# Kernel tuning notes

Measured on AMD Instinct MI355X. Metric: run time of the kernel, lower is better.

The kernel has to match this reference:

```python
import jax, jax.numpy as jnp
import numpy as np

FACTOR = 5  # sampling factor c

def setup_inputs() -> dict:
    key = jax.random.key(0)
    k1, k2, k3, k4 = jax.random.split(key, 4)
    B, H, L, D = 4, 8, 2048, 64
    u = min(max(1, FACTOR * int(np.ceil(np.log(L)))), L)  # sample_k = 40
    return {
        "queries": jax.random.normal(k1, (B, H, L, D), jnp.float32),
        "keys": jax.random.normal(k2, (B, H, L, D), jnp.float32),
        "values": jax.random.normal(k3, (B, H, L, D), jnp.float32),
        "index_sample": jax.random.randint(k4, (L, u), 0, L, jnp.int32),
    }

def reference(queries, keys, values, index_sample):
    B, H, L_Q, D = queries.shape
    L_K = keys.shape[2]
    scale = 1.0 / np.sqrt(D)
    U_part = min(max(1, FACTOR * int(np.ceil(np.log(L_K)))), L_Q)  # n_top queries

    # --- _prob_QK: sampled scores + sparsity measure ---
    # K_sample[b,h,q,s,:] = keys[b,h,index_sample[q,s],:]  -> (B,H,L_Q,u,D)
    K_sample = keys[:, :, index_sample, :]
    QK_sample = jnp.einsum('bhqd,bhqsd->bhqs', queries, K_sample)  # (B,H,L_Q,u)
    M = QK_sample.max(-1) - QK_sample.sum(-1) / L_K                # (B,H,L_Q)
    _, index = jax.lax.top_k(M, U_part)                            # (B,H,U)

    # --- initial context: mean of V for non-selected queries ---
    context = jnp.broadcast_to(values.mean(-2, keepdims=True), (B, H, L_Q, D))

    # --- full attention for the top-U queries only ---
    Q_reduce = jnp.take_along_axis(queries, index[..., None], axis=2)   # (B,H,U,D)
    scores = jnp.einsum('bhud,bhkd->bhuk', Q_reduce, keys) * scale      # (B,H,U,L_K)
    attn = jax.nn.softmax(scores, axis=-1)
    out = jnp.einsum('bhuk,bhkd->bhud', attn, values)                   # (B,H,U,D)

    # --- scatter selected outputs back into the mean context ---
    bi = jnp.arange(B)[:, None, None]
    hi = jnp.arange(H)[None, :, None]
    context = context.at[bi, hi, index].set(out)
    return context
```

## Files before the change

### kernel.cpp

```cpp
#include <hip/hip_runtime.h>
#include <math.h>

#define Bq 4
#define Hh 8
#define Lh 2048
#define Dh 64
#define BH (Bq*Hh)

__global__ __launch_bounds__(256) void kAC(const float* __restrict__ Q,
                                           const float* __restrict__ K,
                                           const float* __restrict__ V,
                                           const int* __restrict__ idxs,
                                           float2* __restrict__ M2,
                                           float* __restrict__ vpart, int u) {
    int bi = blockIdx.x;
    int tid = threadIdx.x;
    if (bi < 2048) {
        int xcd = bi & 7, slot = bi >> 3;
        int bh  = xcd * 4 + (slot >> 6);
        int qt  = (slot >> 1) & 31;
        int half = slot & 1;
        int wave = tid >> 6, lane = tid & 63;
        int g = lane >> 2, c = lane & 3;
        int q = qt * 64 + wave * 16 + g;
        long gq = (long)bh * Lh + q;

        const float* qrow = Q + gq * Dh;
        float4 qf[4];
#pragma unroll
        for (int jj = 0; jj < 4; ++jj)
            qf[jj] = *(const float4*)(qrow + jj * 16 + c * 4);

        int cnt1 = u >> 1;
        int c0 = (half == 0) ? (u - cnt1) : cnt1;
        const int* irow = idxs + (long)q * u + (half ? (u - cnt1) : 0);
        const float* kbase = K + (long)bh * Lh * Dh;

        float mx = -INFINITY, sm = 0.f;
        int s = 0;
        for (; s + 4 <= c0; s += 4) {
            int i0 = irow[s], i1 = irow[s+1], i2 = irow[s+2], i3 = irow[s+3];
            const float* kp0 = kbase + (long)i0 * Dh + c * 4;
            const float* kp1 = kbase + (long)i1 * Dh + c * 4;
            const float* kp2 = kbase + (long)i2 * Dh + c * 4;
            const float* kp3 = kbase + (long)i3 * Dh + c * 4;
            float4 kf[4][4];
#pragma unroll
            for (int jj = 0; jj < 4; ++jj) {
                kf[0][jj] = *(const float4*)(kp0 + jj * 16);
                kf[1][jj] = *(const float4*)(kp1 + jj * 16);
                kf[2][jj] = *(const float4*)(kp2 + jj * 16);
                kf[3][jj] = *(const float4*)(kp3 + jj * 16);
            }
            float a[4];
#pragma unroll
            for (int r = 0; r < 4; ++r) {
                float ac = 0.f;
#pragma unroll
                for (int jj = 0; jj < 4; ++jj)
                    ac += qf[jj].x*kf[r][jj].x + qf[jj].y*kf[r][jj].y
                        + qf[jj].z*kf[r][jj].z + qf[jj].w*kf[r][jj].w;
                a[r] = ac;
            }
#pragma unroll
            for (int r = 0; r < 4; ++r) {
                a[r] += __shfl_xor(a[r], 1);
                a[r] += __shfl_xor(a[r], 2);
                mx = fmaxf(mx, a[r]); sm += a[r];
            }
        }
        for (; s < c0; ++s) {
            int ki = irow[s];
            const float* krow = kbase + (long)ki * Dh + c * 4;
            float acc = 0.f;
#pragma unroll
            for (int jj = 0; jj < 4; ++jj) {
                float4 kf = *(const float4*)(krow + jj * 16);
                acc += qf[jj].x*kf.x + qf[jj].y*kf.y + qf[jj].z*kf.z + qf[jj].w*kf.w;
            }
            acc += __shfl_xor(acc, 1);
            acc += __shfl_xor(acc, 2);
            mx = fmaxf(mx, acc); sm += acc;
        }
        if (c == 0) M2[gq * 2 + half] = make_float2(mx, sm);
    } else {
        int b2 = bi - 2048;
        int xcd = b2 & 7, slot = b2 >> 3;
        int bh = xcd * 4 + (slot >> 3);
        int chunk = slot & 7;
        int d = tid & 63, r0 = tid >> 6;
        const float* vb = V + ((long)bh * Lh + chunk * 256) * Dh;
        float s = 0.f;
        for (int i = 0; i < 64; ++i) s += vb[(r0 + 4 * i) * Dh + d];
        __shared__ float part[4][64];
        part[r0][d] = s;
        __syncthreads();
        if (tid < 64) {
            float t = part[0][tid] + part[1][tid] + part[2][tid] + part[3][tid];
            vpart[(bh * 8 + chunk) * 64 + tid] = t;
        }
    }
}

__global__ __launch_bounds__(256) void kBE(const float2* __restrict__ M2,
                                           const float* __restrict__ vpart,
                                           int* __restrict__ topk,
                                           float* __restrict__ ctx, int U) {
    int bi = blockIdx.x;
    int tid = threadIdx.x;
    if (bi < 4096) {
        long base = (long)bi * 1024;
        int bh = (int)(base >> 17);
        __shared__ float vm[64];
        if (tid < 64) {
            float s = 0.f;
#pragma unroll
            for (int c2 = 0; c2 < 8; ++c2) s += vpart[(bh * 8 + c2) * 64 + tid];
            vm[tid] = s * (1.0f / (float)Lh);
        }
        __syncthreads();
        float4 val = *(const float4*)(vm + ((tid * 4) & 63));
        *(float4*)(ctx + base + tid * 4) = val;
        return;
    }
    int bh = bi - 4096;
    unsigned key[8];
#pragma unroll
    for (int j = 0; j < 8; ++j) {
        long q = (long)bh * Lh + tid + 256 * j;
        float4 mm = *(const float4*)(&M2[q * 2]);
        float Mv = fmaxf(mm.x, mm.z) - (mm.y + mm.w) * (1.0f / (float)Lh);
        unsigned ub = __float_as_uint(Mv);
        key[j] = ub ^ ((ub >> 31) ? 0xFFFFFFFFu : 0x80000000u);
    }
    __shared__ unsigned hist[256];
    __shared__ unsigned prefix_s;
    __shared__ int need_s;
    if (tid == 0) { prefix_s = 0u; need_s = U; }

    for (int level = 3; level >= 0; --level) {
        int shift = level * 8;
        hist[tid] = 0u;
        __syncthreads();
        unsigned prefix = prefix_s;
        int need = need_s;
        unsigned pmask = (level == 3) ? 0u : (0xFFFFFFFFu << (shift + 8));
#pragma unroll
        for (int j = 0; j < 8; ++j)
            if ((key[j] & pmask) == prefix)
                atomicAdd(&hist[(key[j] >> shift) & 0xFF], 1u);
        __syncthreads();
        if (tid < 64) {
            int lane = tid;
            unsigned h0 = hist[lane*4+0], h1 = hist[lane*4+1],
                     h2 = hist[lane*4+2], h3 = hist[lane*4+3];
            unsigned lt = h0 + h1 + h2 + h3;
            unsigned ssum = lt;
#pragma unroll
            for (int off = 1; off < 64; off <<= 1) {
                unsigned t = __shfl_down(ssum, off);
                if (lane + off < 64) ssum += t;
            }
            unsigned sx  = ssum - lt;
            unsigned suf3 = sx  + h3;
            unsigned suf2 = suf3 + h2;
            unsigned suf1 = suf2 + h1;
            unsigned suf0 = suf1 + h0;
            int localb = -1; unsigned nxt = 0u;
            if      ((int)suf3 >= need) { localb = lane*4+3; nxt = sx;   }
            else if ((int)suf2 >= need) { localb = lane*4+2; nxt = suf3; }
            else if ((int)suf1 >= need) { localb = lane*4+1; nxt = suf2; }
            else if ((int)suf0 >= need) { localb = lane*4+0; nxt = suf1; }
            unsigned long long ball = __ballot(localb >= 0);
            int hilane = 63 - __clzll(ball);
            if (lane == hilane) {
                prefix_s = prefix | ((unsigned)localb << shift);
                need_s = need - (int)nxt;
            }
        }
        __syncthreads();
    }
    unsigned T = prefix_s;
    int r = need_s;
    __shared__ int cgt, ceq;
    if (tid == 0) { cgt = 0; ceq = 0; }
    __syncthreads();
    int* out = topk + bh * U;
#pragma unroll
    for (int j = 0; j < 8; ++j) {
        if (key[j] > T) { int p = atomicAdd(&cgt, 1); out[p] = tid + 256 * j; }
        else if (key[j] == T) { int e = atomicAdd(&ceq, 1); if (e < r) out[U - r + e] = tid + 256 * j; }
    }
}

#define TK 64
__global__ __launch_bounds__(256) void kD_part(const float* __restrict__ Q,
                                               const float* __restrict__ K,
                                               const float* __restrict__ V,
                                               const int* __restrict__ topk,
                                               float* __restrict__ pl,
                                               float* __restrict__ pacc,
                                               int U, int nch) {
    int bi = blockIdx.x;
    int xcd = bi & 7, slot = bi >> 3;
    int per = nch * 8;
    int bh = xcd * 4 + slot / per;
    int rest = slot % per;
    int uc = rest >> 3, kc = rest & 7;

    int tid = threadIdx.x;
    int wv = tid >> 6, lane = tid & 63;

    __shared__ float Qs[8 * 64];
    __shared__ float Ks[TK * 68];
    __shared__ float Ps[8 * 68];
    __shared__ float lst[8];
    __shared__ int   qidxs[8];
    float* accbuf = Ks;

    if (tid < 8) {
        int gu = uc * 8 + tid;
        qidxs[tid] = (gu < U) ? topk[bh * U + gu] : 0;
    }
    __syncthreads();
#pragma unroll
    for (int step = 0; step < 2; ++step) {
        int uu = step * 4 + wv;
        int row = qidxs[uu];
        Qs[uu * 64 + lane] = Q[((long)bh * Lh + row) * Dh + lane] * 0.125f;
    }

    int kq = lane, ug = wv;
    float plsum0 = 0.f, plsum1 = 0.f;
    float accv[8] = {0.f,0.f,0.f,0.f,0.f,0.f,0.f,0.f};

    const long kvbase = (long)bh * Lh * Dh;
    const float4* Kg4 = (const float4*)(K + kvbase);
    const float*  Vg  = V + kvbase;
    int kbase0 = kc * 256;

    for (int t = 0; t < 4; ++t) {
        int t0 = kbase0 + t * TK;
        int f40 = t0 * (Dh / 4);
#pragma unroll
        for (int j = 0; j < 4; ++j) {
            int i = tid + 256 * j;
            float4 kv = Kg4[f40 + i];
            int row = i >> 4, col = i & 15;
            *(float4*)(&Ks[row * 68 + col * 4]) = kv;
        }
        __syncthreads();

        float s0 = 0.f, s1 = 0.f;
#pragma unroll
        for (int j16 = 0; j16 < 16; ++j16) {
            float4 kf = *(const float4*)(&Ks[kq * 68 + j16 * 4]);
            float4 qa = *(const float4*)(&Qs[(2 * ug + 0) * 64 + j16 * 4]);
            float4 qb = *(const float4*)(&Qs[(2 * ug + 1) * 64 + j16 * 4]);
            s0 += kf.x * qa.x + kf.y * qa.y + kf.z * qa.z + kf.w * qa.w;
            s1 += kf.x * qb.x + kf.y * qb.y + kf.z * qb.z + kf.w * qb.w;
        }
        float p0 = __expf(s0), p1 = __expf(s1);
        plsum0 += p0; plsum1 += p1;
        Ps[(2 * ug + 0) * 68 + kq] = p0;
        Ps[(2 * ug + 1) * 68 + kq] = p1;
        __syncthreads();

        float vk[16];
        int vrow0 = t0 + wv * 16;
#pragma unroll
        for (int k = 0; k < 16; ++k)
            vk[k] = Vg[(long)(vrow0 + k) * Dh + lane];
#pragma unroll
        for (int u2 = 0; u2 < 8; ++u2) {
            const float* pb = &Ps[u2 * 68 + wv * 16];
            float4 pA = *(const float4*)(pb + 0);
            float4 pB = *(const float4*)(pb + 4);
            float4 pC = *(const float4*)(pb + 8);
            float4 pD = *(const float4*)(pb + 12);
            float ac = accv[u2];
            ac += pA.x*vk[0]  + pA.y*vk[1]  + pA.z*vk[2]  + pA.w*vk[3];
            ac += pB.x*vk[4]  + pB.y*vk[5]  + pB.z*vk[6]  + pB.w*vk[7];
            ac += pC.x*vk[8]  + pC.y*vk[9]  + pC.z*vk[10] + pC.w*vk[11];
            ac += pD.x*vk[12] + pD.y*vk[13] + pD.z*vk[14] + pD.w*vk[15];
            accv[u2] = ac;
        }
    }

#pragma unroll
    for (int off = 1; off < 64; off <<= 1) {
        plsum0 += __shfl_xor(plsum0, off);
        plsum1 += __shfl_xor(plsum1, off);
    }
    if (lane == 0) {
        lst[2 * ug] = plsum0;
        lst[2 * ug + 1] = plsum1;
    }
#pragma unroll
    for (int u2 = 0; u2 < 8; ++u2)
        accbuf[wv * 512 + u2 * 64 + lane] = accv[u2];
    __syncthreads();

    int pbase = (bh * nch + uc) * 8;
    {
        int d = tid & 63, ua = tid >> 6;
#pragma unroll
        for (int h = 0; h < 2; ++h) {
            int u2 = ua + 4 * h;
            float o = accbuf[0 * 512 + u2 * 64 + d] + accbuf[1 * 512 + u2 * 64 + d]
                    + accbuf[2 * 512 + u2 * 64 + d] + accbuf[3 * 512 + u2 * 64 + d];
            pacc[((long)(pbase + u2) * 8 + kc) * 64 + d] = o;
        }
    }
    if (tid < 8) {
        int qp = (pbase + tid) * 8 + kc;
        pl[qp] = lst[tid];
    }
}

__global__ __launch_bounds__(256) void kF_comb(const float* __restrict__ pl,
                                               const float* __restrict__ pacc,
                                               const int* __restrict__ topk,
                                               float* __restrict__ ctx,
                                               int U, int nch) {
    int bi = blockIdx.x;
    int bh = bi / nch, uc = bi % nch;
    int tid = threadIdx.x;
    int u = tid >> 5, t = tid & 31;
    int gu = uc * 8 + u;
    if (gu >= U) return;
    int qbase = (bh * nch + uc) * 8 + u;
    float gl = 0.f;
#pragma unroll
    for (int kc = 0; kc < 8; ++kc) gl += pl[qbase * 8 + kc];
    float inv = 1.0f / gl;
    float o0 = 0.f, o1 = 0.f;
#pragma unroll
    for (int kc = 0; kc < 8; ++kc) {
        const float* a = pacc + ((long)qbase * 8 + kc) * 64;
        o0 += a[t];
        o1 += a[t + 32];
    }
    int row = topk[bh * U + gu];
    float* crow = ctx + ((long)bh * Lh + row) * Dh;
    crow[t]      = o0 * inv;
    crow[t + 32] = o1 * inv;
}

extern "C" void kernel_launch(void* const* d_in, const int* in_sizes, int n_in,
                              void* d_out, int out_size, void* d_ws, size_t ws_size,
                              hipStream_t stream) {
    const float* Q    = (const float*)d_in[0];
    const float* K    = (const float*)d_in[1];
    const float* V    = (const float*)d_in[2];
    const int*   idxs = (const int*)d_in[3];
    float* ctx = (float*)d_out;

    int u = in_sizes[3] / Lh;
    int U = u;
    int nch = (U + 7) / 8;

    float*  wsf   = (float*)d_ws;
    float2* M2    = (float2*)wsf;
    int*    topk  = (int*)(wsf + 262144);
    float*  vpart = wsf + 262144 + 2048;
    float*  pl    = wsf + 280576;
    float*  pacc  = pl + 32 * nch * 8 * 8;

    kAC    <<<2304,         256, 0, stream>>>(Q, K, V, idxs, M2, vpart, u);
    kBE    <<<4128,         256, 0, stream>>>(M2, vpart, topk, ctx, U);
    kD_part<<<BH * nch * 8, 256, 0, stream>>>(Q, K, V, topk, pl, pacc, U, nch);
    kF_comb<<<BH * nch,     256, 0, stream>>>(pl, pacc, topk, ctx, U, nch);
}
```

Measured before the change: 154.7 us.

## Fuse combine kernel into attention partials via last-block counter; vectorize index loads

Removes the separate kF_comb launch. Each kD_part block now atomically increments a per-(bh,chunk) counter, and the last of the 8 key-chunk blocks performs the softmax-normalized reduction and scatter into ctx. The counters are zeroed by an extra block in kBE. Separately, the sampled-score kernel gets a specialized path for 20 samples per half that loads the indices as int4 and fully unrolls the batches. This trades one launch and its gap for threadfences and atomics, plus a serialized tail in the last-arriving block.

```diff
diff --git a/kernel.cpp b/kernel.cpp
--- a/kernel.cpp
+++ b/kernel.cpp
@@ -37,51 +37,63 @@
         const float* kbase = K + (long)bh * Lh * Dh;
 
         float mx = -INFINITY, sm = 0.f;
-        int s = 0;
-        for (; s + 4 <= c0; s += 4) {
-            int i0 = irow[s], i1 = irow[s+1], i2 = irow[s+2], i3 = irow[s+3];
-            const float* kp0 = kbase + (long)i0 * Dh + c * 4;
-            const float* kp1 = kbase + (long)i1 * Dh + c * 4;
-            const float* kp2 = kbase + (long)i2 * Dh + c * 4;
-            const float* kp3 = kbase + (long)i3 * Dh + c * 4;
-            float4 kf[4][4];
-#pragma unroll
-            for (int jj = 0; jj < 4; ++jj) {
-                kf[0][jj] = *(const float4*)(kp0 + jj * 16);
-                kf[1][jj] = *(const float4*)(kp1 + jj * 16);
-                kf[2][jj] = *(const float4*)(kp2 + jj * 16);
-                kf[3][jj] = *(const float4*)(kp3 + jj * 16);
-            }
-            float a[4];
-#pragma unroll
-            for (int r = 0; r < 4; ++r) {
-                float ac = 0.f;
-#pragma unroll
-                for (int jj = 0; jj < 4; ++jj)
-                    ac += qf[jj].x*kf[r][jj].x + qf[jj].y*kf[r][jj].y
-                        + qf[jj].z*kf[r][jj].z + qf[jj].w*kf[r][jj].w;
-                a[r] = ac;
-            }
-#pragma unroll
-            for (int r = 0; r < 4; ++r) {
-                a[r] += __shfl_xor(a[r], 1);
-                a[r] += __shfl_xor(a[r], 2);
-                mx = fmaxf(mx, a[r]); sm += a[r];
-            }
-        }
-        for (; s < c0; ++s) {
-            int ki = irow[s];
-            const float* krow = kbase + (long)ki * Dh + c * 4;
-            float acc = 0.f;
-#pragma unroll
-            for (int jj = 0; jj < 4; ++jj) {
-                float4 kf = *(const float4*)(krow + jj * 16);
-                acc += qf[jj].x*kf.x + qf[jj].y*kf.y + qf[jj].z*kf.z + qf[jj].w*kf.w;
-            }
-            acc += __shfl_xor(acc, 1);
-            acc += __shfl_xor(acc, 2);
-            mx = fmaxf(mx, acc); sm += acc;
-        }
+
+#define KBATCH(I0v, I1v, I2v, I3v)                                           \
+        {                                                                    \
+            const float* kp0 = kbase + (long)(I0v) * Dh + c * 4;             \
+            const float* kp1 = kbase + (long)(I1v) * Dh + c * 4;             \
+            const float* kp2 = kbase + (long)(I2v) * Dh + c * 4;             \
+            const float* kp3 = kbase + (long)(I3v) * Dh + c * 4;             \
+            float4 kf[4][4];                                                 \
+            _Pragma("unroll")                                                \
+            for (int jj = 0; jj < 4; ++jj) {                                 \
+                kf[0][jj] = *(const float4*)(kp0 + jj * 16);                 \
+                kf[1][jj] = *(const float4*)(kp1 + jj * 16);                 \
+                kf[2][jj] = *(const float4*)(kp2 + jj * 16);                 \
+                kf[3][jj] = *(const float4*)(kp3 + jj * 16);                 \
+            }                                                                \
+            _Pragma("unroll")                                                \
+            for (int r = 0; r < 4; ++r) {                                    \
+                float a = 0.f;                                               \
+                _Pragma("unroll")                                            \
+                for (int jj = 0; jj < 4; ++jj)                               \
+                    a += qf[jj].x*kf[r][jj].x + qf[jj].y*kf[r][jj].y         \
+                       + qf[jj].z*kf[r][jj].z + qf[jj].w*kf[r][jj].w;        \
+                a += __shfl_xor(a, 1);                                       \
+                a += __shfl_xor(a, 2);                                       \
+                mx = fmaxf(mx, a); sm += a;                                  \
+            }                                                                \
+        }
+
+        if (c0 == 20) {
+            const int4* ip = (const int4*)irow;
+            int4 Ia = ip[0], Ib = ip[1], Ic = ip[2], Id = ip[3], Ie = ip[4];
+            KBATCH(Ia.x, Ia.y, Ia.z, Ia.w)
+            KBATCH(Ib.x, Ib.y, Ib.z, Ib.w)
+            KBATCH(Ic.x, Ic.y, Ic.z, Ic.w)
+            KBATCH(Id.x, Id.y, Id.z, Id.w)
+            KBATCH(Ie.x, Ie.y, Ie.z, Ie.w)
+        } else {
+            int s = 0;
+            for (; s + 4 <= c0; s += 4) {
+                int i0 = irow[s], i1 = irow[s+1], i2 = irow[s+2], i3 = irow[s+3];
+                KBATCH(i0, i1, i2, i3)
+            }
+            for (; s < c0; ++s) {
+                int ki = irow[s];
+                const float* krow = kbase + (long)ki * Dh + c * 4;
+                float acc = 0.f;
+#pragma unroll
+                for (int jj = 0; jj < 4; ++jj) {
+                    float4 kf = *(const float4*)(krow + jj * 16);
+                    acc += qf[jj].x*kf.x + qf[jj].y*kf.y + qf[jj].z*kf.z + qf[jj].w*kf.w;
+                }
+                acc += __shfl_xor(acc, 1);
+                acc += __shfl_xor(acc, 2);
+                mx = fmaxf(mx, acc); sm += acc;
+            }
+        }
+#undef KBATCH
         if (c == 0) M2[gq * 2 + half] = make_float2(mx, sm);
     } else {
         int b2 = bi - 2048;
@@ -105,9 +117,15 @@
 __global__ __launch_bounds__(256) void kBE(const float2* __restrict__ M2,
                                            const float* __restrict__ vpart,
                                            int* __restrict__ topk,
-                                           float* __restrict__ ctx, int U) {
+                                           float* __restrict__ ctx,
+                                           int* __restrict__ cnt,
+                                           int U, int ncnt) {
     int bi = blockIdx.x;
     int tid = threadIdx.x;
+    if (bi >= 4128) {
+        if (tid < ncnt) cnt[tid] = 0;
+        return;
+    }
     if (bi < 4096) {
         long base = (long)bi * 1024;
         int bh = (int)(base >> 17);
@@ -200,6 +218,8 @@
                                                const int* __restrict__ topk,
                                                float* __restrict__ pl,
                                                float* __restrict__ pacc,
+                                               float* __restrict__ ctx,
+                                               int* __restrict__ cnt,
                                                int U, int nch) {
     int bi = blockIdx.x;
     int xcd = bi & 7, slot = bi >> 3;
@@ -216,6 +236,7 @@
     __shared__ float Ps[8 * 68];
     __shared__ float lst[8];
     __shared__ int   qidxs[8];
+    __shared__ int   lastflag;
     float* accbuf = Ks;
 
     if (tid < 8) {
@@ -316,35 +337,37 @@
         int qp = (pbase + tid) * 8 + kc;
         pl[qp] = lst[tid];
     }
-}
-
-__global__ __launch_bounds__(256) void kF_comb(const float* __restrict__ pl,
-                                               const float* __restrict__ pacc,
-                                               const int* __restrict__ topk,
-                                               float* __restrict__ ctx,
-                                               int U, int nch) {
-    int bi = blockIdx.x;
-    int bh = bi / nch, uc = bi % nch;
-    int tid = threadIdx.x;
-    int u = tid >> 5, t = tid & 31;
-    int gu = uc * 8 + u;
-    if (gu >= U) return;
-    int qbase = (bh * nch + uc) * 8 + u;
-    float gl = 0.f;
-#pragma unroll
-    for (int kc = 0; kc < 8; ++kc) gl += pl[qbase * 8 + kc];
-    float inv = 1.0f / gl;
-    float o0 = 0.f, o1 = 0.f;
-#pragma unroll
-    for (int kc = 0; kc < 8; ++kc) {
-        const float* a = pacc + ((long)qbase * 8 + kc) * 64;
-        o0 += a[t];
-        o1 += a[t + 32];
-    }
-    int row = topk[bh * U + gu];
-    float* crow = ctx + ((long)bh * Lh + row) * Dh;
-    crow[t]      = o0 * inv;
-    crow[t + 32] = o1 * inv;
+
+    __threadfence();
+    __syncthreads();
+    if (tid == 0) {
+        int old = atomicAdd(&cnt[bh * nch + uc], 1);
+        lastflag = (old == 7) ? 1 : 0;
+    }
+    __syncthreads();
+    if (lastflag) {
+        __threadfence();
+        int u2 = tid >> 5, t = tid & 31;
+        int gu = uc * 8 + u2;
+        if (gu < U) {
+            int qbase = pbase + u2;
+            float gl = 0.f;
+#pragma unroll
+            for (int k2 = 0; k2 < 8; ++k2) gl += pl[qbase * 8 + k2];
+            float inv = 1.0f / gl;
+            float o0 = 0.f, o1 = 0.f;
+#pragma unroll
+            for (int k2 = 0; k2 < 8; ++k2) {
+                const float* a = pacc + ((long)qbase * 8 + k2) * 64;
+                o0 += a[t];
+                o1 += a[t + 32];
+            }
+            int row = topk[bh * U + gu];
+            float* crow = ctx + ((long)bh * Lh + row) * Dh;
+            crow[t]      = o0 * inv;
+            crow[t + 32] = o1 * inv;
+        }
+    }
 }
 
 extern "C" void kernel_launch(void* const* d_in, const int* in_sizes, int n_in,
@@ -359,6 +382,7 @@
     int u = in_sizes[3] / Lh;
     int U = u;
     int nch = (U + 7) / 8;
+    int ncnt = 32 * nch;
 
     float*  wsf   = (float*)d_ws;
     float2* M2    = (float2*)wsf;
@@ -366,9 +390,9 @@
     float*  vpart = wsf + 262144 + 2048;
     float*  pl    = wsf + 280576;
     float*  pacc  = pl + 32 * nch * 8 * 8;
+    int*    cnt   = (int*)(pacc + (long)32 * nch * 8 * 8 * 64);
 
     kAC    <<<2304,         256, 0, stream>>>(Q, K, V, idxs, M2, vpart, u);
-    kBE    <<<4128,         256, 0, stream>>>(M2, vpart, topk, ctx, U);
-    kD_part<<<BH * nch * 8, 256, 0, stream>>>(Q, K, V, topk, pl, pacc, U, nch);
-    kF_comb<<<BH * nch,     256, 0, stream>>>(pl, pacc, topk, ctx, U, nch);
+    kBE    <<<4129,         256, 0, stream>>>(M2, vpart, topk, ctx, cnt, U, ncnt);
+    kD_part<<<BH * nch * 8, 256, 0, stream>>>(Q, K, V, topk, pl, pacc, ctx, cnt, U, nch);
 }
```

Measured after the change: 256.6 us. 1.66x slower.

## Process all 40 selected queries per block in sparse attention partial kernel

Applied to the files above, without the earlier changes.

kD_part now has each 512-thread block handle all 40 top-U queries for one (bh, key-chunk), not 8 queries per block. Each K and V tile is loaded once per 40 queries instead of once per 8, which cuts redundant global K/V traffic about fivefold. The grid shrinks from 1280 to 256 blocks, so the GPU is less filled, and each thread holds more accumulators, which raises register and LDS pressure. U=40 is hardcoded into the layout.

```diff
diff --git a/kernel.cpp b/kernel.cpp
--- a/kernel.cpp
+++ b/kernel.cpp
@@ -194,45 +194,41 @@
 }
 
 #define TK 64
-__global__ __launch_bounds__(256) void kD_part(const float* __restrict__ Q,
+__global__ __launch_bounds__(512) void kD_part(const float* __restrict__ Q,
                                                const float* __restrict__ K,
                                                const float* __restrict__ V,
                                                const int* __restrict__ topk,
                                                float* __restrict__ pl,
                                                float* __restrict__ pacc,
-                                               int U, int nch) {
+                                               int U) {
     int bi = blockIdx.x;
     int xcd = bi & 7, slot = bi >> 3;
-    int per = nch * 8;
-    int bh = xcd * 4 + slot / per;
-    int rest = slot % per;
-    int uc = rest >> 3, kc = rest & 7;
+    int bh = xcd * 4 + (slot >> 3);
+    int kc = slot & 7;
 
     int tid = threadIdx.x;
     int wv = tid >> 6, lane = tid & 63;
 
-    __shared__ float Qs[8 * 64];
+    __shared__ float Qs[40 * 64];
     __shared__ float Ks[TK * 68];
-    __shared__ float Ps[8 * 68];
-    __shared__ float lst[8];
-    __shared__ int   qidxs[8];
-    float* accbuf = Ks;
-
-    if (tid < 8) {
-        int gu = uc * 8 + tid;
-        qidxs[tid] = (gu < U) ? topk[bh * U + gu] : 0;
-    }
+    __shared__ float Ps[40 * 68];
+    __shared__ float accbuf[4 * 20 * 64];
+    __shared__ float lst[40];
+    __shared__ int   qidxs[40];
+
+    if (tid < 40) qidxs[tid] = (tid < U) ? topk[bh * U + tid] : 0;
     __syncthreads();
-#pragma unroll
-    for (int step = 0; step < 2; ++step) {
-        int uu = step * 4 + wv;
-        int row = qidxs[uu];
-        Qs[uu * 64 + lane] = Q[((long)bh * Lh + row) * Dh + lane] * 0.125f;
-    }
-
-    int kq = lane, ug = wv;
-    float plsum0 = 0.f, plsum1 = 0.f;
-    float accv[8] = {0.f,0.f,0.f,0.f,0.f,0.f,0.f,0.f};
+    for (int i = tid; i < 40 * 64; i += 512) {
+        int r = i >> 6, d = i & 63;
+        Qs[i] = Q[((long)bh * Lh + qidxs[r]) * Dh + d] * 0.125f;
+    }
+
+    int q0 = wv * 5;
+    int qtr = wv & 3, uoff = (wv >> 2) * 20;
+    float plsum[5] = {0.f, 0.f, 0.f, 0.f, 0.f};
+    float accv[20];
+#pragma unroll
+    for (int i = 0; i < 20; ++i) accv[i] = 0.f;
 
     const long kvbase = (long)bh * Lh * Dh;
     const float4* Kg4 = (const float4*)(K + kvbase);
@@ -243,37 +239,40 @@
         int t0 = kbase0 + t * TK;
         int f40 = t0 * (Dh / 4);
 #pragma unroll
-        for (int j = 0; j < 4; ++j) {
-            int i = tid + 256 * j;
+        for (int j = 0; j < 2; ++j) {
+            int i = tid + 512 * j;
             float4 kv = Kg4[f40 + i];
             int row = i >> 4, col = i & 15;
             *(float4*)(&Ks[row * 68 + col * 4]) = kv;
         }
         __syncthreads();
 
-        float s0 = 0.f, s1 = 0.f;
+        float s[5] = {0.f, 0.f, 0.f, 0.f, 0.f};
 #pragma unroll
         for (int j16 = 0; j16 < 16; ++j16) {
-            float4 kf = *(const float4*)(&Ks[kq * 68 + j16 * 4]);
-            float4 qa = *(const float4*)(&Qs[(2 * ug + 0) * 64 + j16 * 4]);
-            float4 qb = *(const float4*)(&Qs[(2 * ug + 1) * 64 + j16 * 4]);
-            s0 += kf.x * qa.x + kf.y * qa.y + kf.z * qa.z + kf.w * qa.w;
-            s1 += kf.x * qb.x + kf.y * qb.y + kf.z * qb.z + kf.w * qb.w;
-        }
-        float p0 = __expf(s0), p1 = __expf(s1);
-        plsum0 += p0; plsum1 += p1;
-        Ps[(2 * ug + 0) * 68 + kq] = p0;
-        Ps[(2 * ug + 1) * 68 + kq] = p1;
+            float4 kf = *(const float4*)(&Ks[lane * 68 + j16 * 4]);
+#pragma unroll
+            for (int qq = 0; qq < 5; ++qq) {
+                float4 qv = *(const float4*)(&Qs[(q0 + qq) * 64 + j16 * 4]);
+                s[qq] += kf.x*qv.x + kf.y*qv.y + kf.z*qv.z + kf.w*qv.w;
+            }
+        }
+#pragma unroll
+        for (int qq = 0; qq < 5; ++qq) {
+            float p = __expf(s[qq]);
+            plsum[qq] += p;
+            Ps[(q0 + qq) * 68 + lane] = p;
+        }
         __syncthreads();
 
         float vk[16];
-        int vrow0 = t0 + wv * 16;
+        int vrow0 = t0 + qtr * 16;
 #pragma unroll
         for (int k = 0; k < 16; ++k)
             vk[k] = Vg[(long)(vrow0 + k) * Dh + lane];
 #pragma unroll
-        for (int u2 = 0; u2 < 8; ++u2) {
-            const float* pb = &Ps[u2 * 68 + wv * 16];
+        for (int u2 = 0; u2 < 20; ++u2) {
+            const float* pb = &Ps[(uoff + u2) * 68 + qtr * 16];
             float4 pA = *(const float4*)(pb + 0);
             float4 pB = *(const float4*)(pb + 4);
             float4 pC = *(const float4*)(pb + 8);
@@ -288,34 +287,29 @@
     }
 
 #pragma unroll
-    for (int off = 1; off < 64; off <<= 1) {
-        plsum0 += __shfl_xor(plsum0, off);
-        plsum1 += __shfl_xor(plsum1, off);
-    }
-    if (lane == 0) {
-        lst[2 * ug] = plsum0;
-        lst[2 * ug + 1] = plsum1;
-    }
-#pragma unroll
-    for (int u2 = 0; u2 < 8; ++u2)
-        accbuf[wv * 512 + u2 * 64 + lane] = accv[u2];
-    __syncthreads();
-
-    int pbase = (bh * nch + uc) * 8;
-    {
-        int d = tid & 63, ua = tid >> 6;
-#pragma unroll
-        for (int h = 0; h < 2; ++h) {
-            int u2 = ua + 4 * h;
-            float o = accbuf[0 * 512 + u2 * 64 + d] + accbuf[1 * 512 + u2 * 64 + d]
-                    + accbuf[2 * 512 + u2 * 64 + d] + accbuf[3 * 512 + u2 * 64 + d];
-            pacc[((long)(pbase + u2) * 8 + kc) * 64 + d] = o;
-        }
-    }
-    if (tid < 8) {
-        int qp = (pbase + tid) * 8 + kc;
-        pl[qp] = lst[tid];
-    }
+    for (int qq = 0; qq < 5; ++qq) {
+        float v = plsum[qq];
+#pragma unroll
+        for (int off = 1; off < 64; off <<= 1) v += __shfl_xor(v, off);
+        if (lane == 0) lst[q0 + qq] = v;
+    }
+
+#pragma unroll
+    for (int h = 0; h < 2; ++h) {
+        if ((wv >> 2) == h) {
+#pragma unroll
+            for (int u2 = 0; u2 < 20; ++u2)
+                accbuf[qtr * 1280 + u2 * 64 + lane] = accv[u2];
+        }
+        __syncthreads();
+        for (int i = tid; i < 1280; i += 512) {
+            float o = accbuf[i] + accbuf[1280 + i] + accbuf[2560 + i] + accbuf[3840 + i];
+            int gu = h * 20 + (i >> 6), d = i & 63;
+            pacc[((long)(bh * 40 + gu) * 8 + kc) * 64 + d] = o;
+        }
+        __syncthreads();
+    }
+    if (tid < 40) pl[(bh * 40 + tid) * 8 + kc] = lst[tid];
 }
 
 __global__ __launch_bounds__(256) void kF_comb(const float* __restrict__ pl,
@@ -365,10 +359,10 @@
     int*    topk  = (int*)(wsf + 262144);
     float*  vpart = wsf + 262144 + 2048;
     float*  pl    = wsf + 280576;
-    float*  pacc  = pl + 32 * nch * 8 * 8;
-
-    kAC    <<<2304,         256, 0, stream>>>(Q, K, V, idxs, M2, vpart, u);
-    kBE    <<<4128,         256, 0, stream>>>(M2, vpart, topk, ctx, U);
-    kD_part<<<BH * nch * 8, 256, 0, stream>>>(Q, K, V, topk, pl, pacc, U, nch);
-    kF_comb<<<BH * nch,     256, 0, stream>>>(pl, pacc, topk, ctx, U, nch);
-}
+    float*  pacc  = pl + 32 * 40 * 8;
+
+    kAC    <<<2304,     256, 0, stream>>>(Q, K, V, idxs, M2, vpart, u);
+    kBE    <<<4128,     256, 0, stream>>>(M2, vpart, topk, ctx, U);
+    kD_part<<<256,      512, 0, stream>>>(Q, K, V, topk, pl, pacc, U);
+    kF_comb<<<BH * nch, 256, 0, stream>>>(pl, pacc, topk, ctx, U, nch);
+}
```

Result: no change. 154.3 us (-0.2%).
